# Kernel tuning notes

Measured on AMD Instinct MI355X. Metric: run time of the kernel, lower is better.

Reference implementation:

```python
import jax, jax.numpy as jnp
import numpy as np

IN_DIM = 64
OUT_DIM = 64
BN_EPS = 1e-5


def setup_inputs() -> dict:
    key = jax.random.key(0)
    ks = jax.random.split(key, 8)
    B, N, D, O = 8, 512, IN_DIM, OUT_DIM
    s_in = 1.0 / np.sqrt(D)
    x = jax.random.normal(ks[0], (B, N, D), dtype=jnp.float32)
    # torch Linear weights stored as (in, out) so forward is x @ W + b
    W_ap = jax.random.uniform(ks[1], (D, O), jnp.float32, -s_in, s_in)
    b_ap = jnp.zeros((O,), jnp.float32)
    att_w = jax.random.normal(ks[2], (O, 1), jnp.float32) * np.sqrt(2.0 / (O + 1))  # xavier_normal_
    W_pa = jax.random.uniform(ks[3], (D, O), jnp.float32, -s_in, s_in)
    b_pa = jnp.zeros((O,), jnp.float32)
    W_po = jax.random.uniform(ks[4], (D, O), jnp.float32, -s_in, s_in)
    b_po = jnp.zeros((O,), jnp.float32)
    gamma = jnp.ones((O,), jnp.float32)
    beta = jnp.zeros((O,), jnp.float32)
    run_mean = jnp.zeros((O,), jnp.float32)
    run_var = jnp.ones((O,), jnp.float32)
    return {"x": x, "W_ap": W_ap, "b_ap": b_ap, "att_w": att_w,
            "W_pa": W_pa, "b_pa": b_pa, "W_po": W_po, "b_po": b_po,
            "gamma": gamma, "beta": beta, "run_mean": run_mean, "run_var": run_var}


def reference(x, W_ap, b_ap, att_w, W_pa, b_pa, W_po, b_po, gamma, beta, run_mean, run_var):
    # GraphAttentionLayer forward (eval mode: dropout = identity, BN uses running stats)
    # pairwise multiplication of nodes: (b, n, n, d)
    pair = x[:, :, None, :] * x[:, None, :, :]
    # per-pair attention projection + tanh: (b, n, n, o)
    att = jnp.tanh(jnp.einsum('bijd,do->bijo', pair, W_ap) + b_ap)
    # attention-weight vector -> scalar score per pair: (b, n, n, 1)
    scores = att @ att_w
    # softmax over the second node axis (dim=-2 in torch)
    att_map = jax.nn.softmax(scores, axis=-2)[..., 0]  # (b, n, n)
    # attention-weighted aggregation + projections
    agg = jnp.einsum('bij,bjd->bid', att_map, x)
    h = agg @ W_pa + b_pa + (x @ W_po + b_po)
    # BatchNorm1d in inference form
    h = (h - run_mean) * jax.lax.rsqrt(run_var + BN_EPS) * gamma + beta
    return jax.nn.selu(h)
```

## Files before the change

### kernel.cpp

```cpp
#include <hip/hip_runtime.h>
#include <cstdint>

typedef __attribute__((ext_vector_type(8))) short bf16x8;
typedef __attribute__((ext_vector_type(4))) float f32x4;

#if __has_builtin(__builtin_amdgcn_exp2f)
#define EXP2F(x) __builtin_amdgcn_exp2f(x)
#else
#define EXP2F(x) exp2f(x)
#endif
#if __has_builtin(__builtin_amdgcn_rcpf)
#define RCPF(x) __builtin_amdgcn_rcpf(x)
#else
#define RCPF(x) (1.0f/(x))
#endif

#define C2LOG2E 2.885390081777927f
#define LOG2E   1.4426950408889634f

__device__ __forceinline__ unsigned int f2bf(float f) {
    union { float f; unsigned int u; } v; v.f = f;
    return ((v.u + 0x7FFFu + ((v.u >> 16) & 1u)) >> 16);
}
__device__ __forceinline__ float bf2f(unsigned short h) {
    union { unsigned int u; float f; } v; v.u = ((unsigned int)h) << 16; return v.f;
}

__global__ void prep_kernel(const float* __restrict__ x, const float* __restrict__ W_ap,
                            const float* __restrict__ W_pa, const float* __restrict__ W_po,
                            const float* __restrict__ b_pa, const float* __restrict__ b_po,
                            const float* __restrict__ gma, const float* __restrict__ bta,
                            const float* __restrict__ rmean, const float* __restrict__ rvar,
                            unsigned short* __restrict__ Xb, unsigned short* __restrict__ XT,
                            float* __restrict__ Wt,
                            unsigned short* __restrict__ Wpab, unsigned short* __restrict__ Wpob,
                            float* __restrict__ bnA, float* __restrict__ bnBB) {
    int t = blockIdx.x * 256 + threadIdx.x;
    const float* src = x + (size_t)t * 8;
    float4 a = *(const float4*)(src);
    float4 b = *(const float4*)(src + 4);
    unsigned int p0 = f2bf(a.x) | (f2bf(a.y) << 16);
    unsigned int p1 = f2bf(a.z) | (f2bf(a.w) << 16);
    unsigned int p2 = f2bf(b.x) | (f2bf(b.y) << 16);
    unsigned int p3 = f2bf(b.z) | (f2bf(b.w) << 16);
    *(int4*)(Xb + (size_t)t * 8) = make_int4((int)p0, (int)p1, (int)p2, (int)p3);
    {
        int bb = t >> 12;
        int bj = (t >> 3) & 511;
        int d0 = (t & 7) * 8;
        unsigned short* xt = XT + (size_t)bb * (64 * 512) + bj;
        unsigned short e[8] = {(unsigned short)(p0 & 0xffff), (unsigned short)(p0 >> 16),
                               (unsigned short)(p1 & 0xffff), (unsigned short)(p1 >> 16),
                               (unsigned short)(p2 & 0xffff), (unsigned short)(p2 >> 16),
                               (unsigned short)(p3 & 0xffff), (unsigned short)(p3 >> 16)};
        #pragma unroll
        for (int k = 0; k < 8; ++k) xt[(size_t)(d0 + k) * 512] = e[k];
    }
    if (t < 64 * 64) {
        int src_i = (t & 63) * 64 + (t >> 6);
        Wt[t]   = W_ap[src_i];
        Wpab[t] = (unsigned short)f2bf(W_pa[src_i]);
        Wpob[t] = (unsigned short)f2bf(W_po[src_i]);
    }
    if (t < 64) {
        float A = gma[t] * rsqrtf(rvar[t] + 1e-5f);
        bnA[t]  = A;
        bnBB[t] = (b_pa[t] + b_po[t] - rmean[t]) * A + bta[t];
    }
}

__global__ __launch_bounds__(256, 4) void score_kernel(
    const float* __restrict__ x, const float* __restrict__ b_ap, const float* __restrict__ att_w,
    const unsigned short* __restrict__ Xb, const float* __restrict__ Wt,
    unsigned short* __restrict__ E)
{
    const int t  = threadIdx.x;
    const int l  = t & 63;
    const int w  = t >> 6;
    const int bid = blockIdx.x;
    const int b   = bid & 7;
    const int i   = (bid >> 3) * 4 + w;
    const int lm = l & 15;
    const int lq = l >> 4;
    const unsigned short* __restrict__ Xg = Xb + (size_t)b * (512 * 64);
    const float* __restrict__ xi = x + ((size_t)b * 512 + i) * 64;

    bf16x8 af[8];
    #pragma unroll
    for (int ks = 0; ks < 2; ++ks) {
        float4 xc0 = *(const float4*)(xi + ks * 32 + lq * 8);
        float4 xc1 = *(const float4*)(xi + ks * 32 + lq * 8 + 4);
        xc0.x *= C2LOG2E; xc0.y *= C2LOG2E; xc0.z *= C2LOG2E; xc0.w *= C2LOG2E;
        xc1.x *= C2LOG2E; xc1.y *= C2LOG2E; xc1.z *= C2LOG2E; xc1.w *= C2LOG2E;
        #pragma unroll
        for (int of = 0; of < 4; ++of) {
            const float* wr = Wt + (of * 16 + lm) * 64 + ks * 32 + lq * 8;
            float4 w0 = *(const float4*)(wr);
            float4 w1 = *(const float4*)(wr + 4);
            unsigned int p0 = f2bf(w0.x * xc0.x) | (f2bf(w0.y * xc0.y) << 16);
            unsigned int p1 = f2bf(w0.z * xc0.z) | (f2bf(w0.w * xc0.w) << 16);
            unsigned int p2 = f2bf(w1.x * xc1.x) | (f2bf(w1.y * xc1.y) << 16);
            unsigned int p3 = f2bf(w1.z * xc1.z) | (f2bf(w1.w * xc1.w) << 16);
            int4 pk = make_int4((int)p0, (int)p1, (int)p2, (int)p3);
            af[of * 2 + ks] = *reinterpret_cast<bf16x8*>(&pk);
        }
    }

    float n2a[16];
    f32x4 binit[4];
    float asum = 0.f, aabs = 0.f;
    #pragma unroll
    for (int of = 0; of < 4; ++of) {
        #pragma unroll
        for (int r = 0; r < 4; ++r) {
            int o = of * 16 + lq * 4 + r;
            float a = att_w[o];
            n2a[of * 4 + r] = -2.f * a;
            binit[of][r]    = C2LOG2E * b_ap[o];
            asum += a;
            aabs += fabsf(a);
        }
    }
    asum += __shfl_xor(asum, 16); asum += __shfl_xor(asum, 32);
    aabs += __shfl_xor(aabs, 16); aabs += __shfl_xor(aabs, 32);
    const float coff = (asum - aabs) * LOG2E;

    const int it0 = i >> 4;
    const int smax = (it0 < 16) ? 17 : 16;
    unsigned short* __restrict__ Erow = E + ((size_t)b * 512 + i) * 512;
    unsigned short* __restrict__ Ecol = E + (size_t)b * (512 * 512) + i;
    const unsigned short* xrow = Xg + lm * 64 + lq * 8;

    for (int s = 0; s < smax; ++s) {
        const int jt = (it0 + s) & 31;
        bf16x8 b0 = *(const bf16x8*)(xrow + jt * 1024);
        bf16x8 b1 = *(const bf16x8*)(xrow + jt * 1024 + 32);
        f32x4 a0 = binit[0], a1 = binit[1], a2 = binit[2], a3 = binit[3];
        a0 = __builtin_amdgcn_mfma_f32_16x16x32_bf16(af[0], b0, a0, 0, 0, 0);
        a1 = __builtin_amdgcn_mfma_f32_16x16x32_bf16(af[2], b0, a1, 0, 0, 0);
        a2 = __builtin_amdgcn_mfma_f32_16x16x32_bf16(af[4], b0, a2, 0, 0, 0);
        a3 = __builtin_amdgcn_mfma_f32_16x16x32_bf16(af[6], b0, a3, 0, 0, 0);
        a0 = __builtin_amdgcn_mfma_f32_16x16x32_bf16(af[1], b1, a0, 0, 0, 0);
        a1 = __builtin_amdgcn_mfma_f32_16x16x32_bf16(af[3], b1, a1, 0, 0, 0);
        a2 = __builtin_amdgcn_mfma_f32_16x16x32_bf16(af[5], b1, a2, 0, 0, 0);
        a3 = __builtin_amdgcn_mfma_f32_16x16x32_bf16(af[7], b1, a3, 0, 0, 0);
        float ex[16], tt[16];
        #pragma unroll
        for (int r = 0; r < 4; ++r) {
            ex[r]      = EXP2F(a0[r]);
            ex[4 + r]  = EXP2F(a1[r]);
            ex[8 + r]  = EXP2F(a2[r]);
            ex[12 + r] = EXP2F(a3[r]);
        }
        #pragma unroll
        for (int k = 0; k < 16; ++k) tt[k] = RCPF(1.f + ex[k]);
        float q0 = 0.f, q1 = 0.f, q2 = 0.f, q3 = 0.f;
        #pragma unroll
        for (int r = 0; r < 4; ++r) {
            q0 = fmaf(n2a[r],      tt[r],      q0);
            q1 = fmaf(n2a[4 + r],  tt[4 + r],  q1);
            q2 = fmaf(n2a[8 + r],  tt[8 + r],  q2);
            q3 = fmaf(n2a[12 + r], tt[12 + r], q3);
        }
        float ss = (q0 + q1) + (q2 + q3);
        ss += __shfl_xor(ss, 16);
        ss += __shfl_xor(ss, 32);
        float ee = EXP2F(fmaf(ss, LOG2E, coff));
        unsigned short eb = (unsigned short)f2bf(ee);
        if (l < 16) {
            int j = jt * 16 + l;
            Erow[j] = eb;
            if (s != 0) Ecol[(size_t)j * 512] = eb;
        }
    }
}

__global__ __launch_bounds__(256, 4) void agg_kernel(
    const unsigned short* __restrict__ Xb, const unsigned short* __restrict__ XT,
    const unsigned short* __restrict__ E,
    const unsigned short* __restrict__ Wpab, const unsigned short* __restrict__ Wpob,
    const float* __restrict__ bnA, const float* __restrict__ bnBB,
    float* __restrict__ out)
{
    __shared__ float sInv[16];
    __shared__ unsigned short pA[16][72];

    const int t  = threadIdx.x;
    const int l  = t & 63;
    const int w  = t >> 6;
    const int bid = blockIdx.x;
    const int b   = bid & 7;
    const int i0  = (bid >> 3) * 16;
    const int lm = l & 15;
    const int lq = l >> 4;

    const unsigned short* Erow  = E  + ((size_t)b * 512 + i0 + lm) * 512 + lq * 8;
    const unsigned short* xtrow = XT + (size_t)b * (64 * 512) + (w * 16 + lm) * 512 + lq * 8;
    f32x4 acc = (f32x4){0.f, 0.f, 0.f, 0.f};
    float den = 0.f;
    #pragma unroll
    for (int jc = 0; jc < 16; ++jc) {
        bf16x8 ae = *(const bf16x8*)(Erow + jc * 32);
        bf16x8 bx = *(const bf16x8*)(xtrow + jc * 32);
        acc = __builtin_amdgcn_mfma_f32_16x16x32_bf16(ae, bx, acc, 0, 0, 0);
        if (w == 0) {
            #pragma unroll
            for (int e = 0; e < 8; ++e) den += bf2f((unsigned short)ae[e]);
        }
    }
    if (w == 0) {
        den += __shfl_xor(den, 16);
        den += __shfl_xor(den, 32);
        if (l < 16) sInv[l] = RCPF(den);
    }
    #pragma unroll
    for (int r = 0; r < 4; ++r)
        pA[lq * 4 + r][w * 16 + lm] = (unsigned short)f2bf(acc[r]);
    __syncthreads();

    bf16x8 af2[2], afx[2], bwa[2], bwo[2];
    #pragma unroll
    for (int kc = 0; kc < 2; ++kc) {
        af2[kc] = *(const bf16x8*)(&pA[lm][kc * 32 + lq * 8]);
        afx[kc] = *(const bf16x8*)(Xb + ((size_t)b * 512 + i0 + lm) * 64 + kc * 32 + lq * 8);
        bwa[kc] = *(const bf16x8*)(Wpab + (w * 16 + lm) * 64 + kc * 32 + lq * 8);
        bwo[kc] = *(const bf16x8*)(Wpob + (w * 16 + lm) * 64 + kc * 32 + lq * 8);
    }
    f32x4 a2a = (f32x4){0.f, 0.f, 0.f, 0.f};
    f32x4 a2x = (f32x4){0.f, 0.f, 0.f, 0.f};
    a2a = __builtin_amdgcn_mfma_f32_16x16x32_bf16(af2[0], bwa[0], a2a, 0, 0, 0);
    a2x = __builtin_amdgcn_mfma_f32_16x16x32_bf16(afx[0], bwo[0], a2x, 0, 0, 0);
    a2a = __builtin_amdgcn_mfma_f32_16x16x32_bf16(af2[1], bwa[1], a2a, 0, 0, 0);
    a2x = __builtin_amdgcn_mfma_f32_16x16x32_bf16(afx[1], bwo[1], a2x, 0, 0, 0);

    const int o = w * 16 + lm;
    const float A  = bnA[o];
    const float BB = bnBB[o];
    const float alpha = 1.6732632423543772f, scale = 1.0507009873554805f;
    #pragma unroll
    for (int r = 0; r < 4; ++r) {
        int i = i0 + lq * 4 + r;
        float hv = fmaf(sInv[lq * 4 + r], a2a[r], a2x[r]);
        hv = fmaf(hv, A, BB);
        float neg = alpha * (EXP2F(hv * LOG2E) - 1.0f);
        out[((size_t)b * 512 + i) * 64 + o] = scale * (hv > 0.f ? hv : neg);
    }
}

extern "C" void kernel_launch(void* const* d_in, const int* in_sizes, int n_in,
                              void* d_out, int out_size, void* d_ws, size_t ws_size,
                              hipStream_t stream) {
    const float* x     = (const float*)d_in[0];
    const float* W_ap  = (const float*)d_in[1];
    const float* b_ap  = (const float*)d_in[2];
    const float* att_w = (const float*)d_in[3];
    const float* W_pa  = (const float*)d_in[4];
    const float* b_pa  = (const float*)d_in[5];
    const float* W_po  = (const float*)d_in[6];
    const float* b_po  = (const float*)d_in[7];
    const float* gma   = (const float*)d_in[8];
    const float* bta   = (const float*)d_in[9];
    const float* rmean = (const float*)d_in[10];
    const float* rvar  = (const float*)d_in[11];

    char* ws = (char*)d_ws;
    unsigned short* Xb   = (unsigned short*)ws;
    unsigned short* XT   = (unsigned short*)(ws + 512 * 1024);
    float* Wt            = (float*)(ws + 1024 * 1024);
    unsigned short* Wpab = (unsigned short*)(ws + 1040 * 1024);
    unsigned short* Wpob = (unsigned short*)(ws + 1048 * 1024);
    float* bnA           = (float*)(ws + 1056 * 1024);
    float* bnBB          = (float*)(ws + 1057 * 1024);
    unsigned short* E    = (unsigned short*)(ws + 1088 * 1024);
    float* out           = (float*)d_out;

    prep_kernel<<<128, 256, 0, stream>>>(x, W_ap, W_pa, W_po, b_pa, b_po, gma, bta,
                                         rmean, rvar, Xb, XT, Wt, Wpab, Wpob, bnA, bnBB);
    score_kernel<<<1024, 256, 0, stream>>>(x, b_ap, att_w, Xb, Wt, E);
    agg_kernel<<<256, 256, 0, stream>>>(Xb, XT, E, Wpab, Wpob, bnA, bnBB, out);
}
```

Before: 49.51 us.

## Split score rows across two waves and cut register use for higher occupancy

Each row i of the score kernel is now handled by two waves that interleave its j-tiles, and the grid is doubled. Per-lane att_w and bias constants are packed as fp16 pairs. The MFMA output chunks are processed two at a time with zero-initialised accumulators, and the bias is added before exp2. Together these lower VGPR pressure so the launch bound can go from 4 to 8 blocks, aiming for more latency hiding. In exchange the constants lose some precision and there is more per-iteration unpacking work.

```diff
diff --git a/kernel.cpp b/kernel.cpp
--- a/kernel.cpp
+++ b/kernel.cpp
@@ -1,4 +1,5 @@
 #include <hip/hip_runtime.h>
+#include <hip/hip_fp16.h>
 #include <cstdint>
 
 typedef __attribute__((ext_vector_type(8))) short bf16x8;
@@ -24,6 +25,16 @@
 }
 __device__ __forceinline__ float bf2f(unsigned short h) {
     union { unsigned int u; float f; } v; v.u = ((unsigned int)h) << 16; return v.f;
+}
+__device__ __forceinline__ unsigned pack2h(float a, float b) {
+    return (unsigned)__half_as_ushort(__float2half(a)) |
+           ((unsigned)__half_as_ushort(__float2half(b)) << 16);
+}
+__device__ __forceinline__ float h_lo(unsigned u) {
+    return __half2float(__ushort_as_half((unsigned short)(u & 0xffffu)));
+}
+__device__ __forceinline__ float h_hi(unsigned u) {
+    return __half2float(__ushort_as_half((unsigned short)(u >> 16)));
 }
 
 __global__ void prep_kernel(const float* __restrict__ x, const float* __restrict__ W_ap,
@@ -69,7 +80,7 @@
     }
 }
 
-__global__ __launch_bounds__(256, 4) void score_kernel(
+__global__ __launch_bounds__(256, 8) void score_kernel(
     const float* __restrict__ x, const float* __restrict__ b_ap, const float* __restrict__ att_w,
     const unsigned short* __restrict__ Xb, const float* __restrict__ Wt,
     unsigned short* __restrict__ E)
@@ -79,7 +90,8 @@
     const int w  = t >> 6;
     const int bid = blockIdx.x;
     const int b   = bid & 7;
-    const int i   = (bid >> 3) * 4 + w;
+    const int i   = (bid >> 3) * 2 + (w >> 1);
+    const int h   = w & 1;
     const int lm = l & 15;
     const int lq = l >> 4;
     const unsigned short* __restrict__ Xg = Xb + (size_t)b * (512 * 64);
@@ -106,19 +118,18 @@
         }
     }
 
-    float n2a[16];
-    f32x4 binit[4];
+    unsigned n2ap[8], cbp[8];
     float asum = 0.f, aabs = 0.f;
     #pragma unroll
     for (int of = 0; of < 4; ++of) {
         #pragma unroll
-        for (int r = 0; r < 4; ++r) {
-            int o = of * 16 + lq * 4 + r;
-            float a = att_w[o];
-            n2a[of * 4 + r] = -2.f * a;
-            binit[of][r]    = C2LOG2E * b_ap[o];
-            asum += a;
-            aabs += fabsf(a);
+        for (int rp = 0; rp < 2; ++rp) {
+            int o = of * 16 + lq * 4 + rp * 2;
+            float a0 = att_w[o], a1 = att_w[o + 1];
+            n2ap[of * 2 + rp] = pack2h(-2.f * a0, -2.f * a1);
+            cbp[of * 2 + rp]  = pack2h(C2LOG2E * b_ap[o], C2LOG2E * b_ap[o + 1]);
+            asum += a0 + a1;
+            aabs += fabsf(a0) + fabsf(a1);
         }
     }
     asum += __shfl_xor(asum, 16); asum += __shfl_xor(asum, 32);
@@ -131,41 +142,40 @@
     unsigned short* __restrict__ Ecol = E + (size_t)b * (512 * 512) + i;
     const unsigned short* xrow = Xg + lm * 64 + lq * 8;
 
-    for (int s = 0; s < smax; ++s) {
+    for (int s = h; s < smax; s += 2) {
         const int jt = (it0 + s) & 31;
         bf16x8 b0 = *(const bf16x8*)(xrow + jt * 1024);
         bf16x8 b1 = *(const bf16x8*)(xrow + jt * 1024 + 32);
-        f32x4 a0 = binit[0], a1 = binit[1], a2 = binit[2], a3 = binit[3];
-        a0 = __builtin_amdgcn_mfma_f32_16x16x32_bf16(af[0], b0, a0, 0, 0, 0);
-        a1 = __builtin_amdgcn_mfma_f32_16x16x32_bf16(af[2], b0, a1, 0, 0, 0);
-        a2 = __builtin_amdgcn_mfma_f32_16x16x32_bf16(af[4], b0, a2, 0, 0, 0);
-        a3 = __builtin_amdgcn_mfma_f32_16x16x32_bf16(af[6], b0, a3, 0, 0, 0);
-        a0 = __builtin_amdgcn_mfma_f32_16x16x32_bf16(af[1], b1, a0, 0, 0, 0);
-        a1 = __builtin_amdgcn_mfma_f32_16x16x32_bf16(af[3], b1, a1, 0, 0, 0);
-        a2 = __builtin_amdgcn_mfma_f32_16x16x32_bf16(af[5], b1, a2, 0, 0, 0);
-        a3 = __builtin_amdgcn_mfma_f32_16x16x32_bf16(af[7], b1, a3, 0, 0, 0);
-        float ex[16], tt[16];
-        #pragma unroll
-        for (int r = 0; r < 4; ++r) {
-            ex[r]      = EXP2F(a0[r]);
-            ex[4 + r]  = EXP2F(a1[r]);
-            ex[8 + r]  = EXP2F(a2[r]);
-            ex[12 + r] = EXP2F(a3[r]);
-        }
-        #pragma unroll
-        for (int k = 0; k < 16; ++k) tt[k] = RCPF(1.f + ex[k]);
-        float q0 = 0.f, q1 = 0.f, q2 = 0.f, q3 = 0.f;
-        #pragma unroll
-        for (int r = 0; r < 4; ++r) {
-            q0 = fmaf(n2a[r],      tt[r],      q0);
-            q1 = fmaf(n2a[4 + r],  tt[4 + r],  q1);
-            q2 = fmaf(n2a[8 + r],  tt[8 + r],  q2);
-            q3 = fmaf(n2a[12 + r], tt[12 + r], q3);
-        }
-        float ss = (q0 + q1) + (q2 + q3);
-        ss += __shfl_xor(ss, 16);
-        ss += __shfl_xor(ss, 32);
-        float ee = EXP2F(fmaf(ss, LOG2E, coff));
+        float part = 0.f;
+        #pragma unroll
+        for (int ofp = 0; ofp < 2; ++ofp) {
+            f32x4 acc0 = (f32x4){0.f, 0.f, 0.f, 0.f};
+            f32x4 acc1 = (f32x4){0.f, 0.f, 0.f, 0.f};
+            acc0 = __builtin_amdgcn_mfma_f32_16x16x32_bf16(af[(ofp * 2 + 0) * 2 + 0], b0, acc0, 0, 0, 0);
+            acc1 = __builtin_amdgcn_mfma_f32_16x16x32_bf16(af[(ofp * 2 + 1) * 2 + 0], b0, acc1, 0, 0, 0);
+            acc0 = __builtin_amdgcn_mfma_f32_16x16x32_bf16(af[(ofp * 2 + 0) * 2 + 1], b1, acc0, 0, 0, 0);
+            acc1 = __builtin_amdgcn_mfma_f32_16x16x32_bf16(af[(ofp * 2 + 1) * 2 + 1], b1, acc1, 0, 0, 0);
+            float q0 = 0.f, q1 = 0.f;
+            #pragma unroll
+            for (int rp = 0; rp < 2; ++rp) {
+                unsigned uc0 = cbp[(ofp * 2 + 0) * 2 + rp];
+                unsigned uc1 = cbp[(ofp * 2 + 1) * 2 + rp];
+                unsigned un0 = n2ap[(ofp * 2 + 0) * 2 + rp];
+                unsigned un1 = n2ap[(ofp * 2 + 1) * 2 + rp];
+                float e00 = EXP2F(acc0[rp * 2]     + h_lo(uc0));
+                float e01 = EXP2F(acc0[rp * 2 + 1] + h_hi(uc0));
+                float e10 = EXP2F(acc1[rp * 2]     + h_lo(uc1));
+                float e11 = EXP2F(acc1[rp * 2 + 1] + h_hi(uc1));
+                q0 = fmaf(h_lo(un0), RCPF(1.f + e00), q0);
+                q0 = fmaf(h_hi(un0), RCPF(1.f + e01), q0);
+                q1 = fmaf(h_lo(un1), RCPF(1.f + e10), q1);
+                q1 = fmaf(h_hi(un1), RCPF(1.f + e11), q1);
+            }
+            part += q0 + q1;
+        }
+        part += __shfl_xor(part, 16);
+        part += __shfl_xor(part, 32);
+        float ee = EXP2F(fmaf(part, LOG2E, coff));
         unsigned short eb = (unsigned short)f2bf(ee);
         if (l < 16) {
             int j = jt * 16 + l;
@@ -276,6 +286,6 @@
 
     prep_kernel<<<128, 256, 0, stream>>>(x, W_ap, W_pa, W_po, b_pa, b_po, gma, bta,
                                          rmean, rvar, Xb, XT, Wt, Wpab, Wpob, bnA, bnBB);
-    score_kernel<<<1024, 256, 0, stream>>>(x, b_ap, att_w, Xb, Wt, E);
+    score_kernel<<<2048, 256, 0, stream>>>(x, b_ap, att_w, Xb, Wt, E);
     agg_kernel<<<256, 256, 0, stream>>>(Xb, XT, E, Wpab, Wpob, bnA, bnBB, out);
 }
```

After: 119.9 us. +142.3%, slower.
